# Optimization experiments

Hardware: AMD Instinct MI355X
Metric: run time of the kernel (lower is better)

Reference implementation:

```python
import jax, jax.numpy as jnp
import numpy as np

B, S, I, H, C = 32, 512, 768, 512, 10


def setup_inputs() -> dict:
    key = jax.random.key(0)
    ks = jax.random.split(key, 16)
    n = lambda k, shp, s=0.02: jax.random.normal(k, shp, dtype=jnp.float32) * s
    inp = {
        "sentence_embeds": jax.random.normal(ks[0], (B, S, I), dtype=jnp.float32),
        "Wenc": n(ks[1], (H, I)),
        "benc": jnp.zeros((H,), jnp.float32),
        "Wdec": n(ks[2], (H, H)),
        "bdec": jnp.zeros((H,), jnp.float32),
        "v": jax.random.uniform(ks[3], (H,), dtype=jnp.float32),
        "Wih_f": n(ks[4], (4 * H, 2 * I)),
        "Whh_f": n(ks[5], (4 * H, H)),
        "bih_f": jnp.zeros((4 * H,), jnp.float32),
        "bhh_f": jnp.zeros((4 * H,), jnp.float32),
        "Wih_b": n(ks[6], (4 * H, 2 * I)),
        "Whh_b": n(ks[7], (4 * H, H)),
        "bih_b": jnp.zeros((4 * H,), jnp.float32),
        "bhh_b": jnp.zeros((4 * H,), jnp.float32),
        "Wout": n(ks[8], (C, 2 * H)),
        "bout": jnp.zeros((C,), jnp.float32),
    }
    return inp


def _run_direction(embeds, enc_proj, Wdec, bdec, v, Wih, Whh, bih, bhh):
    # embeds: [B,S,I], enc_proj: [B,S,H]. Returns per-step hidden states [S,B,H].
    b = embeds.shape[0]
    h0 = jnp.zeros((b, H), embeds.dtype)
    c0 = jnp.zeros((b, H), embeds.dtype)

    def step(carry, x_t):
        h, c = carry
        # Bahdanau additive attention over all encoder positions
        dec = h @ Wdec.T + bdec                                   # [B,H]
        scores = jnp.einsum("h,bsh->bs", v, jnp.tanh(enc_proj + dec[:, None, :]))
        w = jax.nn.softmax(scores, axis=1)                        # [B,S]
        ctx = jnp.einsum("bs,bsi->bi", w, embeds)                 # [B,I]
        inp = jnp.concatenate([ctx, x_t], axis=1)                 # [B,2I]
        gates = inp @ Wih.T + h @ Whh.T + (bih + bhh)             # [B,4H]
        i, f, g, o = jnp.split(gates, 4, axis=1)                  # torch LSTM gate order
        c = jax.nn.sigmoid(f) * c + jax.nn.sigmoid(i) * jnp.tanh(g)
        h = jax.nn.sigmoid(o) * jnp.tanh(c)
        return (h, c), h

    xs = jnp.swapaxes(embeds, 0, 1)  # [S,B,I]
    _, hs = jax.lax.scan(step, (h0, c0), xs)
    return hs


def reference(sentence_embeds, Wenc, benc, Wdec, bdec, v, Wih_f, Whh_f, bih_f, bhh_f,
              Wih_b, Whh_b, bih_b, bhh_b, Wout, bout):
    # Encoder projection is loop-invariant in the original; compute once.
    enc_proj = sentence_embeds @ Wenc.T + benc  # [B,S,H]
    hs_f = _run_direction(sentence_embeds, enc_proj, Wdec, bdec, v, Wih_f, Whh_f, bih_f, bhh_f)
    hs_b = _run_direction(sentence_embeds[:, ::-1, :], enc_proj, Wdec, bdec, v, Wih_b, Whh_b, bih_b, bhh_b)
    hs_b = hs_b[::-1]                                             # align backward outputs to time order
    combined = jnp.concatenate([hs_f, hs_b], axis=-1)             # [S,B,2H]
    preds = combined @ Wout.T + bout                              # [S,B,C]
    return jnp.swapaxes(preds, 0, 1)                              # [B,S,C]
```

## Files before the change

### kernel.cpp

```cpp
#include <hip/hip_runtime.h>
#include <stdint.h>

#define DEVINL __device__ __forceinline__

constexpr int B_  = 32;
constexpr int S_  = 512;
constexpr int I_  = 768;
constexpr int H_  = 512;
constexpr int C_  = 10;
constexpr int R_  = 64;
constexpr int G4H = 2048;
constexpr int I2_ = 1536;
constexpr int NBLK = 256;
constexpr int NTHR = 512;

using bf16x8 = __attribute__((ext_vector_type(8))) short;
using f32x4  = __attribute__((ext_vector_type(4))) float;
typedef unsigned short u16;
typedef unsigned int   u32;

constexpr size_t OFF_TE   = 0;
constexpr size_t OFF_EMB  = OFF_TE   + (size_t)B_*S_*H_*2;
constexpr size_t OFF_WDEC = OFF_EMB  + (size_t)B_*S_*I_*2;
constexpr size_t OFF_WHH  = OFF_WDEC + (size_t)H_*H_*2;
constexpr size_t OFF_WIL  = OFF_WHH  + (size_t)2*G4H*H_*2;
constexpr size_t OFF_WIR  = OFF_WIL  + (size_t)2*G4H*I_*2;
constexpr size_t OFF_WENC = OFF_WIR  + (size_t)2*G4H*I_*2;
constexpr size_t OFF_H    = OFF_WENC + (size_t)H_*I_*2;
constexpr size_t OFF_C    = OFF_H    + (size_t)R_*H_*2;
constexpr size_t OFF_TD   = OFF_C    + (size_t)R_*H_*4;
constexpr size_t OFF_HWH  = OFF_TD   + (size_t)R_*H_*4;
constexpr size_t OFF_XW   = OFF_HWH  + (size_t)R_*G4H*4;
constexpr size_t OFF_CTX  = OFF_XW   + (size_t)R_*G4H*4;
constexpr size_t OFF_SUME = OFF_CTX  + (size_t)R_*I_*4;
constexpr size_t OFF_M    = OFF_SUME + 256;
constexpr size_t OFF_BAR  = OFF_M    + 256;
constexpr int    BAR_W    = 64 + 32*32;
constexpr size_t WS_NEED  = OFF_BAR + BAR_W*4;

DEVINL float asf(u32 u){ union{u32 i; float f;} x; x.i=u; return x.f; }
DEVINL u32   asu(float f){ union{u32 i; float f;} x; x.f=f; return x.i; }
DEVINL float bf2f(u16 h){ return asf((u32)h << 16); }
DEVINL u16   f2bf(float f){ u32 u = asu(f); return (u16)((u + 0x7fffu + ((u>>16)&1u)) >> 16); }
DEVINL float frcp(float x){
#if __has_builtin(__builtin_amdgcn_rcpf)
  return __builtin_amdgcn_rcpf(x);
#else
  return 1.0f/x;
#endif
}
DEVINL float sigm(float x){ return frcp(1.0f + __expf(-x)); }

DEVINL void gridbar(u32* bar, u32 n){
  __syncthreads();
  if (threadIdx.x == 0){
    __threadfence();
    u32 g = blockIdx.x >> 3;
    u32 old = __hip_atomic_fetch_add(&bar[64 + g*32], 1u, __ATOMIC_RELAXED, __HIP_MEMORY_SCOPE_AGENT);
    if (old == n*8u - 1u){
      u32 r = __hip_atomic_fetch_add(&bar[0], 1u, __ATOMIC_RELAXED, __HIP_MEMORY_SCOPE_AGENT);
      if (r == n*32u - 1u){
        __hip_atomic_store(&bar[32], n, __ATOMIC_RELAXED, __HIP_MEMORY_SCOPE_AGENT);
      }
    }
    while (__hip_atomic_load(&bar[32], __ATOMIC_RELAXED, __HIP_MEMORY_SCOPE_AGENT) < n)
      __builtin_amdgcn_s_sleep(2);
    __threadfence();
  }
  __syncthreads();
}

struct SMemB { float ldsE[2][2][32]; float cpart[4][96][16]; };
struct SMemC { u16 Abuf[16][776]; float Gpre[32][16]; float Gs[32][16];
               float Hb[16][8]; float inv[16]; float sum[16]; };
union alignas(16) SMem { SMemB b; SMemC c; };

__global__ void k_setup(char* ws, const float* Wenc, const float* Wdec,
                        const float* Whh_f, const float* Whh_b,
                        const float* Wih_f, const float* Wih_b,
                        float* out){
  int tid = blockIdx.x*blockDim.x + threadIdx.x;
  int nth = gridDim.x*blockDim.x;
  for (int i = tid; i < B_*S_*C_; i += nth) out[i] = 0.f;
  u16* hB = (u16*)(ws+OFF_H);
  for (int i = tid; i < R_*H_; i += nth) hB[i] = 0;
  float* cS = (float*)(ws+OFF_C);
  for (int i = tid; i < R_*H_; i += nth) cS[i] = 0.f;
  float* mb = (float*)(ws+OFF_M);
  for (int i = tid; i < R_; i += nth) mb[i] = 0.f;
  u32* bar = (u32*)(ws+OFF_BAR);
  for (int i = tid; i < BAR_W; i += nth) bar[i] = 0u;
  u16* wd = (u16*)(ws+OFF_WDEC);
  for (int i = tid; i < H_*H_; i += nth) wd[i] = f2bf(Wdec[i]);
  u16* we = (u16*)(ws+OFF_WENC);
  for (int i = tid; i < H_*I_; i += nth) we[i] = f2bf(Wenc[i]);
  u16* wh = (u16*)(ws+OFF_WHH);
  for (int i = tid; i < G4H*H_; i += nth){
    wh[i] = f2bf(Whh_f[i]);
    wh[G4H*H_ + i] = f2bf(Whh_b[i]);
  }
  u16* wl = (u16*)(ws+OFF_WIL);
  u16* wr = (u16*)(ws+OFF_WIR);
  for (int i = tid; i < G4H*I_; i += nth){
    int n = i / I_, k = i - n*I_;
    wl[i]            = f2bf(Wih_f[n*I2_ + k]);
    wr[i]            = f2bf(Wih_f[n*I2_ + I_ + k]);
    wl[G4H*I_ + i]   = f2bf(Wih_b[n*I2_ + k]);
    wr[G4H*I_ + i]   = f2bf(Wih_b[n*I2_ + I_ + k]);
  }
}

__global__ void k_embconv(char* ws, const float* emb){
  u16* e = (u16*)(ws+OFF_EMB);
  int tid = blockIdx.x*blockDim.x + threadIdx.x;
  int nth = gridDim.x*blockDim.x;
  int n4 = (B_*S_*I_)/4;
  const float4* src = (const float4*)emb;
  ushort4* dst = (ushort4*)e;
  for (int i = tid; i < n4; i += nth){
    float4 x = src[i];
    ushort4 o;
    o.x = f2bf(x.x); o.y = f2bf(x.y); o.z = f2bf(x.z); o.w = f2bf(x.w);
    dst[i] = o;
  }
}

__global__ __launch_bounds__(256) void k_enc(char* ws, const float* benc){
  const u16* A = (const u16*)(ws+OFF_EMB);
  const u16* W = (const u16*)(ws+OFF_WENC);
  u16* Te = (u16*)(ws+OFF_TE);
  int wg = blockIdx.x;
  int mt = wg >> 3, ng = wg & 7;
  int wave = threadIdx.x >> 6, lane = threadIdx.x & 63;
  int m0 = mt*16, n0 = ng*64 + wave*16;
  int lr = lane & 15, lkb = (lane>>4)*8;
  const u16* ap = A + (size_t)(m0+lr)*I_ + lkb;
  const u16* bp = W + (size_t)(n0+lr)*I_ + lkb;
  f32x4 acc = {0.f,0.f,0.f,0.f};
  for (int k = 0; k < I_; k += 32){
    bf16x8 a = *(const bf16x8*)(ap + k);
    bf16x8 b = *(const bf16x8*)(bp + k);
    acc = __builtin_amdgcn_mfma_f32_16x16x32_bf16(a, b, acc, 0, 0, 0);
  }
  int row4 = (lane>>4)*4;
  #pragma unroll
  for (int q = 0; q < 4; q++){
    int rr = m0 + row4 + q, cc = n0 + lr;
    Te[(size_t)rr*H_ + cc] = f2bf(tanhf(acc[q] + benc[cc]));
  }
}

__global__ __launch_bounds__(NTHR) void k_persist(char* ws,
        const float* bdec, const float* v,
        const float* bih_f, const float* bhh_f,
        const float* bih_b, const float* bhh_b,
        const float* Wout, const float* bout, float* out){
  __shared__ SMem sh;
  __shared__ alignas(16) u16 wWhh[16][520];
  __shared__ alignas(16) u16 wWIR[16][776];
  __shared__ alignas(16) u16 wDec[16][520];
  __shared__ alignas(16) u16 wWIL[32][776];
  __shared__ float wOutL[10][8];
  __shared__ float bsumL[32];
  u32* bar = (u32*)(ws+OFF_BAR);
  u32 gen = 0;
  const int tid = threadIdx.x, lane = tid & 63, wave = tid >> 6;
  const int lr = lane & 15, lkb = (lane>>4)*8, row4 = (lane>>4)*4;
  const int blk = blockIdx.x;
  const int dirA = blk & 1, n0A = blk >> 1;
  const int ab   = blk & 31, pair = blk >> 5;
  const int s0A  = pair*32, s0B = S_ - pair*32 - 32;
  const int h0   = lane*8;
  const int cg   = (tid < 384) ? (tid % 96) : 0;
  const int rq   = (tid < 384) ? (tid / 96) : 0;
  const int dirC = blk >> 7, ncC = (blk >> 1) & 63, qbC = blk & 1;

  { const u16* src = (const u16*)(ws+OFF_WHH) + (size_t)dirA*G4H*H_ + (size_t)n0A*16*H_;
    for (int idx = tid; idx < 16*64; idx += NTHR){ int r = idx>>6, c8 = idx&63;
      *(uint4*)&wWhh[r][c8*8] = *(const uint4*)(src + (size_t)r*H_ + c8*8); } }
  { const u16* src = (const u16*)(ws+OFF_WIR) + (size_t)dirA*G4H*I_ + (size_t)n0A*16*I_;
    for (int idx = tid; idx < 16*96; idx += NTHR){ int r = idx/96, c8 = idx - r*96;
      *(uint4*)&wWIR[r][c8*8] = *(const uint4*)(src + (size_t)r*I_ + c8*8); } }
  if (blk < 32){
    const u16* src = (const u16*)(ws+OFF_WDEC) + (size_t)blk*16*H_;
    for (int idx = tid; idx < 16*64; idx += NTHR){ int r = idx>>6, c8 = idx&63;
      *(uint4*)&wDec[r][c8*8] = *(const uint4*)(src + (size_t)r*H_ + c8*8); } }
  { const u16* src = (const u16*)(ws+OFF_WIL) + (size_t)dirC*G4H*I_;
    for (int idx = tid; idx < 32*96; idx += NTHR){ int pr = idx/96, c8 = idx - pr*96;
      int g = pr>>3, j = pr&7;
      *(uint4*)&wWIL[pr][c8*8] = *(const uint4*)(src + (size_t)(g*512 + ncC*8 + j)*I_ + c8*8); } }
  { const float* bihp = dirC ? bih_b : bih_f;
    const float* bhhp = dirC ? bhh_b : bhh_f;
    if (tid < 32){ int g = tid>>3, c = tid&7; int n = g*512 + ncC*8 + c;
      bsumL[tid] = bihp[n] + bhhp[n]; }
    if (tid >= 64 && tid < 144){ int q = tid-64; int cc = q>>3, c = q&7;
      wOutL[cc][c] = Wout[(size_t)cc*1024 + dirC*512 + ncC*8 + c]; } }
  bf16x8 teR[8];
  { const u16* Te = (const u16*)(ws+OFF_TE);
    #pragma unroll
    for (int k = 0; k < 8; ++k){
      int r = wave + 8*k; int ci = r >> 5, u = r & 31;
      int s = (ci ? s0B : s0A) + u;
      teR[k] = *(const bf16x8*)(Te + ((size_t)(ab*S_ + s))*H_ + h0); } }
  bf16x8 embR[16];
  if (tid < 384){
    const u16* E = (const u16*)(ws+OFF_EMB);
    #pragma unroll
    for (int j = 0; j < 16; ++j){
      int r = rq*16 + j;
      int s = (r < 32) ? (s0A + r) : (s0B + (r - 32));
      embR[j] = *(const bf16x8*)(E + ((size_t)(ab*S_ + s))*I_ + cg*8); } }
  __syncthreads();

  for (int t = 0; t < S_; ++t){
    {
      const u16* hB = (const u16*)(ws+OFF_H);
      if (wave < 2){
        int m0 = dirA*32 + wave*16;
        const u16* ap = hB + (size_t)(m0+lr)*H_ + lkb;
        f32x4 acc = {0.f,0.f,0.f,0.f};
        for (int k = 0; k < H_; k += 32){
          bf16x8 a = *(const bf16x8*)(ap + k);
          bf16x8 b = *(const bf16x8*)(&wWhh[lr][k + lkb]);
          acc = __builtin_amdgcn_mfma_f32_16x16x32_bf16(a, b, acc, 0, 0, 0);
        }
        float* o = (float*)(ws+OFF_HWH);
        #pragma unroll
        for (int q = 0; q < 4; q++)
          o[(size_t)(m0 + row4 + q)*G4H + n0A*16 + lr] = acc[q];
      } else if (wave < 4){
        int bbase = (wave-2)*16;
        int trow = dirA ? (S_-1-t) : t;
        const u16* E = (const u16*)(ws+OFF_EMB);
        const u16* ap = E + ((size_t)(bbase+lr)*S_ + trow)*I_ + lkb;
        f32x4 acc = {0.f,0.f,0.f,0.f};
        for (int k = 0; k < I_; k += 32){
          bf16x8 a = *(const bf16x8*)(ap + k);
          bf16x8 b = *(const bf16x8*)(&wWIR[lr][k + lkb]);
          acc = __builtin_amdgcn_mfma_f32_16x16x32_bf16(a, b, acc, 0, 0, 0);
        }
        float* o = (float*)(ws+OFF_XW);
        #pragma unroll
        for (int q = 0; q < 4; q++)
          o[(size_t)(dirA*32 + bbase + row4 + q)*G4H + n0A*16 + lr] = acc[q];
      } else if (blk < 32){
        int m0 = (wave-4)*16;
        const u16* ap = hB + (size_t)(m0+lr)*H_ + lkb;
        f32x4 acc = {0.f,0.f,0.f,0.f};
        for (int k = 0; k < H_; k += 32){
          bf16x8 a = *(const bf16x8*)(ap + k);
          bf16x8 b = *(const bf16x8*)(&wDec[lr][k + lkb]);
          acc = __builtin_amdgcn_mfma_f32_16x16x32_bf16(a, b, acc, 0, 0, 0);
        }
        float* Td = (float*)(ws+OFF_TD);
        #pragma unroll
        for (int q = 0; q < 4; q++){
          int rr = m0 + row4 + q, cc = blk*16 + lr;
          Td[rr*H_ + cc] = tanhf(acc[q] + bdec[cc]);
        }
      } else {
        int zid = (((blk-32)<<2) + (wave-4))*64 + lane;
        float* ctx = (float*)(ws+OFF_CTX);
        if (zid < R_*I_) ctx[zid] = 0.f;
        if (zid < R_) ((float*)(ws+OFF_SUME))[zid] = 0.f;
      }
    }
    gridbar(bar, ++gen);
    {
      const float* Td = (const float*)(ws+OFF_TD);
      const float* mbp = (const float*)(ws+OFF_M);
      float tdf[8], tdb[8], va[8];
      #pragma unroll
      for (int j = 0; j < 8; j++){
        tdf[j] = Td[ab*H_ + h0 + j];
        tdb[j] = Td[(32+ab)*H_ + h0 + j];
        va[j]  = v[h0 + j];
      }
      float mF = mbp[ab], mB = mbp[32+ab];
      #pragma unroll
      for (int k = 0; k < 8; ++k){
        int r = wave + 8*k;
        int ci = r >> 5, u = r & 31;
        bf16x8 tv = teR[k];
        float af = 0.f, ab2 = 0.f;
        #pragma unroll
        for (int j = 0; j < 8; ++j){
          float te = bf2f((u16)tv[j]);
          float df = fmaf(te, tdf[j], 1.0f);
          float db = fmaf(te, tdb[j], 1.0f);
          af  = fmaf((te+tdf[j])*frcp(df), va[j], af);
          ab2 = fmaf((te+tdb[j])*frcp(db), va[j], ab2);
        }
        #pragma unroll
        for (int off = 1; off < 64; off <<= 1){
          af  += __shfl_xor(af, off);
          ab2 += __shfl_xor(ab2, off);
        }
        float ef = __expf(fminf(fmaxf(af  - mF, -80.f), 80.f));
        float eb = __expf(fminf(fmaxf(ab2 - mB, -80.f), 80.f));
        if (lane == 0){ sh.b.ldsE[0][ci][u] = ef; sh.b.ldsE[1][ci][u] = eb; }
      }
      __syncthreads();
      if (tid < 2){
        float s = 0.f;
        for (int ci = 0; ci < 2; ci++)
          for (int u = 0; u < 32; u++) s += sh.b.ldsE[tid][ci][u];
        atomicAdd((float*)(ws+OFF_SUME) + tid*32 + ab, s);
      }
      if (tid < 384){
        const int ci = rq >> 1;
        float cf[8] = {0,0,0,0,0,0,0,0}, cb[8] = {0,0,0,0,0,0,0,0};
        #pragma unroll
        for (int j = 0; j < 16; ++j){
          int u = ((rq & 1) << 4) + j;
          float wf = sh.b.ldsE[0][ci][u];
          float wb = sh.b.ldsE[1][1-ci][31-u];
          bf16x8 e = embR[j];
          #pragma unroll
          for (int x = 0; x < 8; ++x){
            float ev = bf2f((u16)e[x]);
            cf[x] = fmaf(wf, ev, cf[x]);
            cb[x] = fmaf(wb, ev, cb[x]);
          }
        }
        #pragma unroll
        for (int x = 0; x < 8; ++x){
          sh.b.cpart[rq][cg][x]   = cf[x];
          sh.b.cpart[rq][cg][8+x] = cb[x];
        }
      }
      __syncthreads();
      {
        float* ctxg = (float*)(ws+OFF_CTX);
        for (int o = tid; o < 1536; o += NTHR){
          int d = (o >= 768) ? 1 : 0;
          int col = o - d*768;
          int cgx = col >> 3, c = col & 7;
          float s = sh.b.cpart[0][cgx][d*8+c] + sh.b.cpart[1][cgx][d*8+c]
                  + sh.b.cpart[2][cgx][d*8+c] + sh.b.cpart[3][cgx][d*8+c];
          atomicAdd(&ctxg[(size_t)(d*32+ab)*I_ + col], s);
        }
      }
    }
    gridbar(bar, ++gen);
    {
      const float* se = (const float*)(ws+OFF_SUME) + dirC*32 + qbC*16;
      if (tid < 16){
        float s_ = se[tid];
        sh.c.sum[tid] = s_;
        sh.c.inv[tid] = 1.0f / fmaxf(s_, 1e-30f);
      }
      __syncthreads();
      const float* ctx = (const float*)(ws+OFF_CTX) + (size_t)(dirC*32 + qbC*16)*I_;
      for (int idx = tid; idx < 16*I_; idx += NTHR){
        int j = idx / I_, k = idx - j*I_;
        sh.c.Abuf[j][k] = f2bf(ctx[(size_t)j*I_ + k] * sh.c.inv[j]);
      }
      __syncthreads();
      f32x4 acc = {0.f,0.f,0.f,0.f};
      if (wave < 2){
        for (int k = 0; k < I_; k += 32){
          bf16x8 av = *(const bf16x8*)(&sh.c.Abuf[lr][k + lkb]);
          bf16x8 bv = *(const bf16x8*)(&wWIL[wave*16 + lr][k + lkb]);
          acc = __builtin_amdgcn_mfma_f32_16x16x32_bf16(av, bv, acc, 0, 0, 0);
        }
      } else {
        const float* xW = (const float*)(ws+OFF_XW);
        const float* hW = (const float*)(ws+OFF_HWH);
        for (int ii = tid - 128; ii < 512; ii += 384){
          int pr = ii >> 4, j = ii & 15;
          int g = pr >> 3, c = pr & 7;
          int n = g*512 + ncC*8 + c;
          size_t rr = (size_t)(dirC*32 + qbC*16 + j);
          sh.c.Gpre[pr][j] = xW[rr*G4H + n] + hW[rr*G4H + n] + bsumL[pr];
        }
      }
      __syncthreads();
      if (wave < 2){
        int pr = wave*16 + lr;
        #pragma unroll
        for (int q = 0; q < 4; q++){
          int j = row4 + q;
          sh.c.Gs[pr][j] = acc[q] + sh.c.Gpre[pr][j];
        }
      }
      __syncthreads();
      float* cS = (float*)(ws+OFF_C);
      u16* hBw = (u16*)(ws+OFF_H);
      if (tid < 128){
        int j = tid >> 3, c = tid & 7;
        int hg = ncC*8 + c;
        size_t rr = (size_t)(dirC*32 + qbC*16 + j);
        float ig = sigm(sh.c.Gs[c][j]);
        float fg = sigm(sh.c.Gs[8+c][j]);
        float gg = tanhf(sh.c.Gs[16+c][j]);
        float og = sigm(sh.c.Gs[24+c][j]);
        float cn = fmaf(fg, cS[rr*H_ + hg], ig*gg);
        float hn = og * tanhf(cn);
        cS[rr*H_ + hg] = cn;
        hBw[rr*H_ + hg] = f2bf(hn);
        sh.c.Hb[j][c] = hn;
      }
      __syncthreads();
      if (tid < 160){
        int j = tid/10, cc = tid - j*10;
        float s = 0.f;
        #pragma unroll
        for (int c = 0; c < 8; c++) s = fmaf(sh.c.Hb[j][c], wOutL[cc][c], s);
        if (dirC == 0 && ncC == 0) s += bout[cc];
        int bb = qbC*16 + j;
        int st = dirC ? (S_-1-t) : t;
        atomicAdd(&out[((size_t)bb*S_ + st)*C_ + cc], s);
      }
      if (ncC == 0 && tid < 16){
        float* mbp = (float*)(ws+OFF_M);
        mbp[dirC*32 + qbC*16 + tid] += logf(fmaxf(sh.c.sum[tid], 1e-30f));
      }
    }
    gridbar(bar, ++gen);
  }
}

extern "C" void kernel_launch(void* const* d_in, const int* in_sizes, int n_in,
                              void* d_out, int out_size, void* d_ws, size_t ws_size,
                              hipStream_t stream){
  const float* emb   = (const float*)d_in[0];
  const float* Wenc  = (const float*)d_in[1];
  const float* benc  = (const float*)d_in[2];
  const float* Wdec  = (const float*)d_in[3];
  const float* bdec  = (const float*)d_in[4];
  const float* v     = (const float*)d_in[5];
  const float* Wih_f = (const float*)d_in[6];
  const float* Whh_f = (const float*)d_in[7];
  const float* bih_f = (const float*)d_in[8];
  const float* bhh_f = (const float*)d_in[9];
  const float* Wih_b = (const float*)d_in[10];
  const float* Whh_b = (const float*)d_in[11];
  const float* bih_b = (const float*)d_in[12];
  const float* bhh_b = (const float*)d_in[13];
  const float* Wout  = (const float*)d_in[14];
  const float* bout  = (const float*)d_in[15];
  float* out = (float*)d_out;
  char* ws = (char*)d_ws;
  if (ws_size < WS_NEED) return;

  k_setup<<<dim3(512), dim3(256), 0, stream>>>(ws, Wenc, Wdec, Whh_f, Whh_b, Wih_f, Wih_b, out);
  k_embconv<<<dim3(2048), dim3(256), 0, stream>>>(ws, emb);
  k_enc<<<dim3(8192), dim3(256), 0, stream>>>(ws, benc);
  k_persist<<<dim3(NBLK), dim3(NTHR), 0, stream>>>(ws, bdec, v,
      bih_f, bhh_f, bih_b, bhh_b, Wout, bout, out);
}
```

Before: 27.48 ms.

## Replace grid-barrier fences with agent-scope relaxed atomics on cross-block data

Drops the __threadfence calls from the software grid barrier. In their place, every cross-block shared value (hidden state, gate partials, Td, ctx, sums, running max) is read and written with agent-scope relaxed atomic loads and stores, so the data bypasses non-coherent caches. The hidden state is now packed into 32-bit words and loaded in batched registers, and the ctx load is restructured into a per-thread contiguous batch. The goal is to cut the cost of the full-cache fences paid three times per timestep. The risk is memory-ordering correctness, because relaxed atomics with no fence may not guarantee visibility ordering relative to the barrier counter.

```diff
diff --git a/kernel.cpp b/kernel.cpp
--- a/kernel.cpp
+++ b/kernel.cpp
@@ -51,10 +51,15 @@
 }
 DEVINL float sigm(float x){ return frcp(1.0f + __expf(-x)); }
 
+DEVINL float ldc_f(const float* p){ return __hip_atomic_load(p, __ATOMIC_RELAXED, __HIP_MEMORY_SCOPE_AGENT); }
+DEVINL void  stc_f(float* p, float v){ __hip_atomic_store(p, v, __ATOMIC_RELAXED, __HIP_MEMORY_SCOPE_AGENT); }
+DEVINL u32   ldc_u(const u32* p){ return __hip_atomic_load(p, __ATOMIC_RELAXED, __HIP_MEMORY_SCOPE_AGENT); }
+DEVINL void  stc_u(u32* p, u32 v){ __hip_atomic_store(p, v, __ATOMIC_RELAXED, __HIP_MEMORY_SCOPE_AGENT); }
+DEVINL void  addc_f(float* p, float v){ __hip_atomic_fetch_add(p, v, __ATOMIC_RELAXED, __HIP_MEMORY_SCOPE_AGENT); }
+
 DEVINL void gridbar(u32* bar, u32 n){
   __syncthreads();
   if (threadIdx.x == 0){
-    __threadfence();
     u32 g = blockIdx.x >> 3;
     u32 old = __hip_atomic_fetch_add(&bar[64 + g*32], 1u, __ATOMIC_RELAXED, __HIP_MEMORY_SCOPE_AGENT);
     if (old == n*8u - 1u){
@@ -65,9 +70,28 @@
     }
     while (__hip_atomic_load(&bar[32], __ATOMIC_RELAXED, __HIP_MEMORY_SCOPE_AGENT) < n)
       __builtin_amdgcn_s_sleep(2);
-    __threadfence();
   }
   __syncthreads();
+}
+
+DEVINL f32x4 gemm_h16(const u32* h32, size_t base, const u16 (*W)[520], int lr, int lkb){
+  f32x4 acc = {0.f,0.f,0.f,0.f};
+  #pragma unroll
+  for (int half = 0; half < 2; ++half){
+    u32 hreg[32];
+    #pragma unroll
+    for (int i2 = 0; i2 < 32; ++i2)
+      hreg[i2] = ldc_u(h32 + base + half*128 + (i2>>2)*16 + (i2&3));
+    #pragma unroll
+    for (int ki = 0; ki < 8; ++ki){
+      union { bf16x8 v; u32 w[4]; } ua;
+      ua.w[0]=hreg[ki*4+0]; ua.w[1]=hreg[ki*4+1];
+      ua.w[2]=hreg[ki*4+2]; ua.w[3]=hreg[ki*4+3];
+      bf16x8 b = *(const bf16x8*)(&W[lr][(half*8+ki)*32 + lkb]);
+      acc = __builtin_amdgcn_mfma_f32_16x16x32_bf16(ua.v, b, acc, 0, 0, 0);
+    }
+  }
+  return acc;
 }
 
 struct SMemB { float ldsE[2][2][32]; float cpart[4][96][16]; };
@@ -214,20 +238,15 @@
 
   for (int t = 0; t < S_; ++t){
     {
-      const u16* hB = (const u16*)(ws+OFF_H);
+      const u32* h32 = (const u32*)(ws+OFF_H);
       if (wave < 2){
         int m0 = dirA*32 + wave*16;
-        const u16* ap = hB + (size_t)(m0+lr)*H_ + lkb;
-        f32x4 acc = {0.f,0.f,0.f,0.f};
-        for (int k = 0; k < H_; k += 32){
-          bf16x8 a = *(const bf16x8*)(ap + k);
-          bf16x8 b = *(const bf16x8*)(&wWhh[lr][k + lkb]);
-          acc = __builtin_amdgcn_mfma_f32_16x16x32_bf16(a, b, acc, 0, 0, 0);
-        }
+        size_t base = (((size_t)(m0+lr))*H_ + lkb) >> 1;
+        f32x4 acc = gemm_h16(h32, base, wWhh, lr, lkb);
         float* o = (float*)(ws+OFF_HWH);
         #pragma unroll
         for (int q = 0; q < 4; q++)
-          o[(size_t)(m0 + row4 + q)*G4H + n0A*16 + lr] = acc[q];
+          stc_f(&o[(size_t)(m0 + row4 + q)*G4H + n0A*16 + lr], acc[q]);
       } else if (wave < 4){
         int bbase = (wave-2)*16;
         int trow = dirA ? (S_-1-t) : t;
@@ -242,27 +261,22 @@
         float* o = (float*)(ws+OFF_XW);
         #pragma unroll
         for (int q = 0; q < 4; q++)
-          o[(size_t)(dirA*32 + bbase + row4 + q)*G4H + n0A*16 + lr] = acc[q];
+          stc_f(&o[(size_t)(dirA*32 + bbase + row4 + q)*G4H + n0A*16 + lr], acc[q]);
       } else if (blk < 32){
         int m0 = (wave-4)*16;
-        const u16* ap = hB + (size_t)(m0+lr)*H_ + lkb;
-        f32x4 acc = {0.f,0.f,0.f,0.f};
-        for (int k = 0; k < H_; k += 32){
-          bf16x8 a = *(const bf16x8*)(ap + k);
-          bf16x8 b = *(const bf16x8*)(&wDec[lr][k + lkb]);
-          acc = __builtin_amdgcn_mfma_f32_16x16x32_bf16(a, b, acc, 0, 0, 0);
-        }
+        size_t base = (((size_t)(m0+lr))*H_ + lkb) >> 1;
+        f32x4 acc = gemm_h16(h32, base, wDec, lr, lkb);
         float* Td = (float*)(ws+OFF_TD);
         #pragma unroll
         for (int q = 0; q < 4; q++){
           int rr = m0 + row4 + q, cc = blk*16 + lr;
-          Td[rr*H_ + cc] = tanhf(acc[q] + bdec[cc]);
+          stc_f(&Td[rr*H_ + cc], tanhf(acc[q] + bdec[cc]));
         }
       } else {
         int zid = (((blk-32)<<2) + (wave-4))*64 + lane;
         float* ctx = (float*)(ws+OFF_CTX);
-        if (zid < R_*I_) ctx[zid] = 0.f;
-        if (zid < R_) ((float*)(ws+OFF_SUME))[zid] = 0.f;
+        if (zid < R_*I_) stc_f(&ctx[zid], 0.f);
+        if (zid < R_) stc_f((float*)(ws+OFF_SUME) + zid, 0.f);
       }
     }
     gridbar(bar, ++gen);
@@ -272,11 +286,11 @@
       float tdf[8], tdb[8], va[8];
       #pragma unroll
       for (int j = 0; j < 8; j++){
-        tdf[j] = Td[ab*H_ + h0 + j];
-        tdb[j] = Td[(32+ab)*H_ + h0 + j];
+        tdf[j] = ldc_f(&Td[ab*H_ + h0 + j]);
+        tdb[j] = ldc_f(&Td[(32+ab)*H_ + h0 + j]);
         va[j]  = v[h0 + j];
       }
-      float mF = mbp[ab], mB = mbp[32+ab];
+      float mF = ldc_f(&mbp[ab]), mB = ldc_f(&mbp[32+ab]);
       #pragma unroll
       for (int k = 0; k < 8; ++k){
         int r = wave + 8*k;
@@ -305,7 +319,7 @@
         float s = 0.f;
         for (int ci = 0; ci < 2; ci++)
           for (int u = 0; u < 32; u++) s += sh.b.ldsE[tid][ci][u];
-        atomicAdd((float*)(ws+OFF_SUME) + tid*32 + ab, s);
+        addc_f((float*)(ws+OFF_SUME) + tid*32 + ab, s);
       }
       if (tid < 384){
         const int ci = rq >> 1;
@@ -338,7 +352,7 @@
           int cgx = col >> 3, c = col & 7;
           float s = sh.b.cpart[0][cgx][d*8+c] + sh.b.cpart[1][cgx][d*8+c]
                   + sh.b.cpart[2][cgx][d*8+c] + sh.b.cpart[3][cgx][d*8+c];
-          atomicAdd(&ctxg[(size_t)(d*32+ab)*I_ + col], s);
+          addc_f(&ctxg[(size_t)(d*32+ab)*I_ + col], s);
         }
       }
     }
@@ -346,15 +360,22 @@
     {
       const float* se = (const float*)(ws+OFF_SUME) + dirC*32 + qbC*16;
       if (tid < 16){
-        float s_ = se[tid];
+        float s_ = ldc_f(&se[tid]);
         sh.c.sum[tid] = s_;
         sh.c.inv[tid] = 1.0f / fmaxf(s_, 1e-30f);
       }
       __syncthreads();
-      const float* ctx = (const float*)(ws+OFF_CTX) + (size_t)(dirC*32 + qbC*16)*I_;
-      for (int idx = tid; idx < 16*I_; idx += NTHR){
-        int j = idx / I_, k = idx - j*I_;
-        sh.c.Abuf[j][k] = f2bf(ctx[(size_t)j*I_ + k] * sh.c.inv[j]);
+      {
+        const float* ctx = (const float*)(ws+OFF_CTX) + (size_t)(dirC*32 + qbC*16)*I_;
+        float creg[24];
+        int j = tid >> 5, k0 = (tid & 31) * 24;
+        #pragma unroll
+        for (int i2 = 0; i2 < 24; ++i2)
+          creg[i2] = ldc_f(ctx + (size_t)j*I_ + k0 + i2);
+        float inv = sh.c.inv[j];
+        #pragma unroll
+        for (int i2 = 0; i2 < 24; ++i2)
+          sh.c.Abuf[j][k0 + i2] = f2bf(creg[i2] * inv);
       }
       __syncthreads();
       f32x4 acc = {0.f,0.f,0.f,0.f};
@@ -372,7 +393,7 @@
           int g = pr >> 3, c = pr & 7;
           int n = g*512 + ncC*8 + c;
           size_t rr = (size_t)(dirC*32 + qbC*16 + j);
-          sh.c.Gpre[pr][j] = xW[rr*G4H + n] + hW[rr*G4H + n] + bsumL[pr];
+          sh.c.Gpre[pr][j] = ldc_f(&xW[rr*G4H + n]) + ldc_f(&hW[rr*G4H + n]) + bsumL[pr];
         }
       }
       __syncthreads();
@@ -386,7 +407,6 @@
       }
       __syncthreads();
       float* cS = (float*)(ws+OFF_C);
-      u16* hBw = (u16*)(ws+OFF_H);
       if (tid < 128){
         int j = tid >> 3, c = tid & 7;
         int hg = ncC*8 + c;
@@ -398,10 +418,15 @@
         float cn = fmaf(fg, cS[rr*H_ + hg], ig*gg);
         float hn = og * tanhf(cn);
         cS[rr*H_ + hg] = cn;
-        hBw[rr*H_ + hg] = f2bf(hn);
         sh.c.Hb[j][c] = hn;
       }
       __syncthreads();
+      if (tid < 64){
+        int j = tid >> 2, cp = tid & 3;
+        size_t rr = (size_t)(dirC*32 + qbC*16 + j);
+        u32 pk = (u32)f2bf(sh.c.Hb[j][cp*2]) | ((u32)f2bf(sh.c.Hb[j][cp*2+1]) << 16);
+        stc_u((u32*)(ws+OFF_H) + ((rr*H_ + ncC*8) >> 1) + cp, pk);
+      }
       if (tid < 160){
         int j = tid/10, cc = tid - j*10;
         float s = 0.f;
@@ -413,8 +438,8 @@
         atomicAdd(&out[((size_t)bb*S_ + st)*C_ + cc], s);
       }
       if (ncC == 0 && tid < 16){
-        float* mbp = (float*)(ws+OFF_M);
-        mbp[dirC*32 + qbC*16 + tid] += logf(fmaxf(sh.c.sum[tid], 1e-30f));
+        float* mp = (float*)(ws+OFF_M) + dirC*32 + qbC*16 + tid;
+        stc_f(mp, ldc_f(mp) + logf(fmaxf(sh.c.sum[tid], 1e-30f)));
       }
     }
     gridbar(bar, ++gen);
```

Result: faster. 26.21 ms (-4.6%).
